# Kernel tuning notes

Measured on AMD Instinct MI355X. Metric: run time of the kernel, lower is better.

Reference implementation:

```python
import jax, jax.numpy as jnp
import numpy as np

SCORE_THRESH = 0.05
NMS_THRESH = 0.5
DETS_PER_IMG = 100
IMG_W, IMG_H = 1333.0, 800.0
BBOX_XFORM_CLIP = float(np.log(1000.0 / 16.0))
WX, WY, WW, WH = 10.0, 10.0, 5.0, 5.0


def decode_boxes(rel, ref):
    widths = ref[:, 2] - ref[:, 0] + 1.0
    heights = ref[:, 3] - ref[:, 1] + 1.0
    ctr_x = ref[:, 0] + 0.5 * widths
    ctr_y = ref[:, 1] + 0.5 * heights
    dx = rel[:, 0] / WX
    dy = rel[:, 1] / WY
    dw = jnp.minimum(rel[:, 2] / WW, BBOX_XFORM_CLIP)
    dh = jnp.minimum(rel[:, 3] / WH, BBOX_XFORM_CLIP)
    pcx = dx * widths + ctr_x
    pcy = dy * heights + ctr_y
    pw = jnp.exp(dw) * widths
    ph = jnp.exp(dh) * heights
    return jnp.stack([pcx - 0.5 * pw, pcy - 0.5 * ph,
                      pcx + 0.5 * pw - 1.0, pcy + 0.5 * ph - 1.0], axis=1)


def pairwise_iou(b):
    # torchvision-style IoU (no +1), b: [n,4] xyxy
    area = (b[:, 2] - b[:, 0]) * (b[:, 3] - b[:, 1])
    lt = jnp.maximum(b[:, None, :2], b[None, :, :2])
    rb = jnp.minimum(b[:, None, 2:], b[None, :, 2:])
    wh = jnp.clip(rb - lt, 0.0)
    inter = wh[..., 0] * wh[..., 1]
    return inter / (area[:, None] + area[None, :] - inter + 1e-12)


def nms_keep(boxes, scores, valid):
    # masked greedy NMS; returns boolean keep mask in original order
    n = boxes.shape[0]
    order = jnp.argsort(-jnp.where(valid, scores, -jnp.inf))
    b = boxes[order]
    v = valid[order]
    iou = pairwise_iou(b)  # [n,n]
    idx = jnp.arange(n)

    def body(i, keep):
        suppressed = jnp.any(keep & (iou[i] > NMS_THRESH) & (idx < i))
        return keep.at[i].set(v[i] & ~suppressed)

    keep_sorted = jax.lax.fori_loop(0, n, body, jnp.zeros(n, dtype=bool))
    return jnp.zeros(n, dtype=bool).at[order].set(keep_sorted)


def setup_inputs() -> dict:
    key = jax.random.key(0)
    k1, k2, k3, k4, k5 = jax.random.split(key, 5)
    C, K = 16, 2048
    class_logit = jax.random.normal(k1, (C * K, 2), jnp.float32)
    box_regression = jax.random.normal(k2, (C * K, 8), jnp.float32) * 0.5
    x1 = jax.random.uniform(k3, (K,)) * (IMG_W - 220.0)
    y1 = jax.random.uniform(k4, (K,)) * (IMG_H - 220.0)
    wh = 20.0 + jax.random.uniform(k5, (K, 2)) * 180.0
    proposal_boxes = jnp.stack([x1, y1, x1 + wh[:, 0], y1 + wh[:, 1]], axis=1).astype(jnp.float32)
    unique_labels = jnp.arange(1, C + 1, dtype=jnp.int32)
    return {"class_logit": class_logit, "box_regression": box_regression,
            "proposal_boxes": proposal_boxes, "unique_labels": unique_labels}


def reference(class_logit, box_regression, proposal_boxes, unique_labels):
    C = unique_labels.shape[0]
    K = proposal_boxes.shape[0]
    # softmax over binary logits, take foreground prob
    prob = jax.nn.softmax(class_logit, axis=1)[:, 1]  # [C*K]
    rel = box_regression[:, 4:8]
    ref_boxes = jnp.tile(proposal_boxes, (C, 1))  # class-major [C*K,4]
    dec = decode_boxes(rel, ref_boxes)
    # clip_to_image (remove_empty=False), TO_REMOVE = 1
    dec = jnp.stack([jnp.clip(dec[:, 0], 0.0, IMG_W - 1.0),
                     jnp.clip(dec[:, 1], 0.0, IMG_H - 1.0),
                     jnp.clip(dec[:, 2], 0.0, IMG_W - 1.0),
                     jnp.clip(dec[:, 3], 0.0, IMG_H - 1.0)], axis=1)
    boxes_c = dec.reshape(C, K, 4)
    scores_c = prob.reshape(C, K)
    valid = scores_c > SCORE_THRESH
    keep = jax.vmap(nms_keep)(boxes_c, scores_c, valid).reshape(-1)  # [C*K]
    flat_scores = scores_c.reshape(-1)
    n_det = jnp.sum(keep)
    masked = jnp.where(keep, flat_scores, -jnp.inf)
    kth = jax.lax.top_k(masked, DETS_PER_IMG)[0][-1]  # 100th largest kept score
    keep_final = jnp.where(n_det > DETS_PER_IMG, keep & (flat_scores >= kth), keep)
    labels = jnp.broadcast_to(unique_labels[:, None], (C, K)).reshape(-1)
    out_boxes = jnp.where(keep_final[:, None], dec, 0.0)
    out_scores = jnp.where(keep_final, flat_scores, 0.0)
    out5 = jnp.concatenate([out_boxes, out_scores[:, None]], axis=1)  # [C*K,5]
    return out5, labels, keep_final
```

## Files before the change

kernel.cpp:

```cpp
#include <hip/hip_runtime.h>
#include <hip/hip_bf16.h>

#define NCLS 16
#define NBOX 2048
#define NTOT (NCLS * NBOX)
#define NCHUNK 32
#define SCORE_THRESH 0.05f
#define NMS_THRESH 0.5f
#define DETS_PER_IMG 100
#define BBOX_CLIP 4.135166556742356f

typedef unsigned long long u64;

__device__ __forceinline__ u64 sel_mx(u64 a, u64 b, bool keepmax) {
    u64 mx = (a > b) ? a : b;
    u64 mn = (a > b) ? b : a;
    return keepmax ? mx : mn;
}

__global__ __launch_bounds__(1024) void sortdecode_kernel(
    const float* __restrict__ logits,
    const float* __restrict__ regr,
    const float* __restrict__ props,
    float4* __restrict__ dec,
    u64* __restrict__ keys_out,
    float4* __restrict__ sbox4)
{
    int c = blockIdx.x;
    int tid = threadIdx.x;
    int w = tid >> 6, l = tid & 63;
    int p0 = w * 128 + l;
    int p1 = p0 + 64;
    __shared__ u64 sk[NBOX];

    u64 e01[2];
#pragma unroll
    for (int s = 0; s < 2; s++) {
#pragma clang fp contract(off)
        int t = s ? p1 : p0;
        int i = c * NBOX + t;
        float x0 = logits[2 * i + 0];
        float x1 = logits[2 * i + 1];
        float m = fmaxf(x0, x1);
        float e0f = expf(x0 - m);
        float e1f = expf(x1 - m);
        float score = e1f / (e0f + e1f);

        float px1 = props[4 * t + 0];
        float py1 = props[4 * t + 1];
        float px2 = props[4 * t + 2];
        float py2 = props[4 * t + 3];

        float bw = px2 - px1 + 1.0f;
        float bh = py2 - py1 + 1.0f;
        float cx = px1 + 0.5f * bw;
        float cy = py1 + 0.5f * bh;

        float dx = regr[8 * i + 4] / 10.0f;
        float dy = regr[8 * i + 5] / 10.0f;
        float dw = fminf(regr[8 * i + 6] / 5.0f, BBOX_CLIP);
        float dh = fminf(regr[8 * i + 7] / 5.0f, BBOX_CLIP);

        float pcx = dx * bw + cx;
        float pcy = dy * bh + cy;
        float pw  = expf(dw) * bw;
        float ph  = expf(dh) * bh;

        float b0 = pcx - 0.5f * pw;
        float b1 = pcy - 0.5f * ph;
        float b2 = pcx + 0.5f * pw - 1.0f;
        float b3 = pcy + 0.5f * ph - 1.0f;

        b0 = fminf(fmaxf(b0, 0.0f), 1332.0f);
        b1 = fminf(fmaxf(b1, 0.0f), 799.0f);
        b2 = fminf(fmaxf(b2, 0.0f), 1332.0f);
        b3 = fminf(fmaxf(b3, 0.0f), 799.0f);

        dec[i] = make_float4(b0, b1, b2, b3);

        unsigned mono = 0u;
        if (score > SCORE_THRESH) mono = __float_as_uint(score) | 0x80000000u;
        e01[s] = ((u64)mono << 32) | (u64)(unsigned)(NBOX - 1 - t);
    }
    u64 e0 = e01[0], e1 = e01[1];

    for (int k = 2; k <= NBOX; k <<= 1) {
        bool desc0 = (p0 & k) == 0;
        bool desc1 = (p1 & k) == 0;
        for (int j = k >> 1; j > 0; j >>= 1) {
            if (j >= 128) {
                sk[p0] = e0; sk[p1] = e1;
                __syncthreads();
                u64 q0 = sk[p0 ^ j];
                u64 q1 = sk[p1 ^ j];
                e0 = sel_mx(e0, q0, desc0 ^ ((p0 & j) != 0));
                e1 = sel_mx(e1, q1, desc1 ^ ((p1 & j) != 0));
                __syncthreads();
            } else if (j == 64) {
                u64 mx = (e0 > e1) ? e0 : e1;
                u64 mn = (e0 > e1) ? e1 : e0;
                e0 = desc0 ? mx : mn;
                e1 = desc0 ? mn : mx;
            } else {
                u64 q0 = __shfl_xor(e0, j);
                u64 q1 = __shfl_xor(e1, j);
                bool hi = (l & j) != 0;
                e0 = sel_mx(e0, q0, desc0 ^ hi);
                e1 = sel_mx(e1, q1, desc1 ^ hi);
            }
        }
    }

    sk[p0] = e0; sk[p1] = e1;
    __syncthreads();

    for (int t = tid; t < NBOX; t += 1024) {
        u64 key = sk[t];
        keys_out[c * NBOX + t] = key;
        int idx = (NBOX - 1) - (int)(key & 0xFFFFFFFFull);
        int orig = c * NBOX + idx;
        sbox4[c * NBOX + t] = dec[orig];
    }
}

__global__ __launch_bounds__(1024) void mask_kernel(
    const float4* __restrict__ sbox4,
    u64* __restrict__ maskT)
{
    int c = blockIdx.x >> 4;
    int p = blockIdx.x & 15;
    __shared__ float4 box[NBOX];

    for (int i = threadIdx.x; i < NBOX; i += 1024)
        box[i] = sbox4[c * NBOX + i];
    __syncthreads();

    int r = threadIdx.x & 63;
    int g = threadIdx.x >> 6;

    for (int pass = 0; pass < 2; pass++) {
#pragma clang fp contract(off)
        int Jc = pass ? (31 - p) : p;
        int j = Jc * 64 + r;
        float4 jb = box[j];
        float jar = (jb.z - jb.x) * (jb.w - jb.y);
        float hj = 0.5f * jar;
        float colC = hj + 5e-13f;

        for (int I = g; I <= Jc; I += 16) {
            u64 w = 0;
            int rbase = I * 64;
#pragma unroll
            for (int i2 = 0; i2 < 64; i2++) {
#pragma clang fp contract(off)
                int gi = rbase + i2;
                float4 rb = box[gi];
                float ar = (rb.z - rb.x) * (rb.w - rb.y);
                float rha = 0.5f * ar;
                float lx = fmaxf(rb.x, jb.x);
                float ly = fmaxf(rb.y, jb.y);
                float rx = fminf(rb.z, jb.z);
                float ry = fminf(rb.w, jb.w);
                float ww = fmaxf(rx - lx, 0.0f);
                float hh = fmaxf(ry - ly, 0.0f);
                float inter = ww * hh;
                float s  = rha + colC;
                float band = 2e-6f * s;
                float delta = fmaf(1.5f, inter, -s);
                bool over = delta > band;
                bool amb = fabsf(delta) <= band;
                if (__any(amb)) {
                    float un = ar + jar - inter + 1e-12f;
                    float iou = inter / un;
                    bool ovx = iou > NMS_THRESH;
                    over = amb ? ovx : over;
                }
                if (over) w |= 1ull << i2;
            }
            if (I == Jc) w &= (1ull << r) - 1ull;
            maskT[((size_t)c * NCHUNK + I) * NBOX + j] = w;
        }
    }
}

__global__ __launch_bounds__(64) void resolve_kernel(
    const u64* __restrict__ keys,
    const u64* __restrict__ maskT,
    unsigned* __restrict__ keepbits)
{
    int c = blockIdx.x;
    int l = threadIdx.x;
    const u64* MT = maskT + (size_t)c * NCHUNK * NBOX;
    const u64* K  = keys + (size_t)c * NBOX;

    unsigned sup = 0;
    u64 tm[2][NCHUNK - 1];

#pragma unroll
    for (int t = 0; t < NCHUNK - 1; t++)
        tm[0][t] = MT[(size_t)(1 + t) * 64 + l];
    u64 diag = MT[l];
    u64 key  = K[l];

#pragma unroll
    for (int I = 0; I < NCHUNK; I++) {
        u64 diagN = diag, keyN = key;
        if (I + 1 < NCHUNK) {
            const u64* rowpN = MT + (size_t)(I + 1) * NBOX + l;
#pragma unroll
            for (int t = 0; t < NCHUNK - 2 - I; t++)
                tm[(I + 1) & 1][t] = rowpN[(size_t)(I + 2 + t) * 64];
            diagN = MT[(size_t)(I + 1) * NBOX + (size_t)(I + 1) * 64 + l];
            keyN  = K[(I + 1) * 64 + l];
        }
        __builtin_amdgcn_sched_barrier(0);

        unsigned mono = (unsigned)(key >> 32);
        bool av = (mono != 0u) && (((sup >> I) & 1u) == 0u);
        u64 kept = 0;
        u64 availB = __ballot(av);
        while (availB) {
            u64 front = __ballot(av && ((diag & availB) == 0ull));
            kept |= front;
            bool fr = ((front >> l) & 1ull) != 0ull;
            bool sp = ((diag & front) != 0ull);
            av = av && !fr && !sp;
            availB = __ballot(av);
        }

        int idx = (NBOX - 1) - (int)(key & 0xFFFFFFFFull);
        keepbits[c * NBOX + idx] = ((kept >> l) & 1ull) ? (mono & 0x7FFFFFFFu) : 0u;

#pragma unroll
        for (int t = 0; t < NCHUNK - 1 - I; t++)
            sup |= (tm[I & 1][t] & kept) ? (1u << (I + 1 + t)) : 0u;

        diag = diagN;
        key  = keyN;
    }
}

__global__ __launch_bounds__(1024) void select_kernel(
    const unsigned* __restrict__ keepbits,
    int* __restrict__ stats)
{
    __shared__ int hist[4][2048];
    __shared__ int gsum[64];
    __shared__ int s_cnt;
    __shared__ unsigned s_prefix;
    __shared__ int s_rank;
    int tid = threadIdx.x;
    int cw = (tid >> 6) & 3;
    int* h0 = &hist[0][0];
    const uint4* kb4 = (const uint4*)keepbits;

    for (int b = tid; b < 4 * 2048; b += 1024) h0[b] = 0;
    if (tid == 0) s_cnt = 0;
    __syncthreads();
    int cnt = 0;
    for (int i = tid; i < NTOT / 4; i += 1024) {
        uint4 v = kb4[i];
        if (v.x) { cnt++; atomicAdd(&hist[cw][v.x >> 21], 1); }
        if (v.y) { cnt++; atomicAdd(&hist[cw][v.y >> 21], 1); }
        if (v.z) { cnt++; atomicAdd(&hist[cw][v.z >> 21], 1); }
        if (v.w) { cnt++; atomicAdd(&hist[cw][v.w >> 21], 1); }
    }
#pragma unroll
    for (int off = 32; off > 0; off >>= 1) cnt += __shfl_down(cnt, off);
    if ((tid & 63) == 0) atomicAdd(&s_cnt, cnt);
    __syncthreads();
    for (int b = tid; b < 2048; b += 1024)
        h0[b] = hist[0][b] + hist[1][b] + hist[2][b] + hist[3][b];
    __syncthreads();
    int n_det = s_cnt;

    if (n_det > DETS_PER_IMG) {
        if (tid < 64) {
            int s = 0;
            for (int t = 0; t < 32; t++) s += h0[tid * 32 + t];
            gsum[tid] = s;
        }
        __syncthreads();
        if (tid == 0) {
            int r = DETS_PER_IMG;
            int g = 63;
            for (; g > 0; g--) { if (r <= gsum[g]) break; r -= gsum[g]; }
            int b = g * 32 + 31;
            for (; b > g * 32; b--) { if (r <= h0[b]) break; r -= h0[b]; }
            s_prefix = (unsigned)b << 21;
            s_rank = r;
        }
        __syncthreads();

        unsigned p1 = s_prefix;
        for (int b = tid; b < 2048; b += 1024) h0[b] = 0;
        __syncthreads();
        for (int i = tid; i < NTOT / 4; i += 1024) {
            uint4 v = kb4[i];
            if (v.x && (v.x >> 21 << 21) == p1) atomicAdd(&h0[(v.x >> 10) & 2047], 1);
            if (v.y && (v.y >> 21 << 21) == p1) atomicAdd(&h0[(v.y >> 10) & 2047], 1);
            if (v.z && (v.z >> 21 << 21) == p1) atomicAdd(&h0[(v.z >> 10) & 2047], 1);
            if (v.w && (v.w >> 21 << 21) == p1) atomicAdd(&h0[(v.w >> 10) & 2047], 1);
        }
        __syncthreads();
        if (tid < 64) {
            int s = 0;
            for (int t = 0; t < 32; t++) s += h0[tid * 32 + t];
            gsum[tid] = s;
        }
        __syncthreads();
        if (tid == 0) {
            int r = s_rank;
            int g = 63;
            for (; g > 0; g--) { if (r <= gsum[g]) break; r -= gsum[g]; }
            int b = g * 32 + 31;
            for (; b > g * 32; b--) { if (r <= h0[b]) break; r -= h0[b]; }
            s_prefix = p1 | ((unsigned)b << 10);
            s_rank = r;
        }
        __syncthreads();

        unsigned p2 = s_prefix;
        for (int b = tid; b < 1024; b += 1024) h0[b] = 0;
        __syncthreads();
        for (int i = tid; i < NTOT / 4; i += 1024) {
            uint4 v = kb4[i];
            if (v.x && (v.x >> 10 << 10) == p2) atomicAdd(&h0[v.x & 1023], 1);
            if (v.y && (v.y >> 10 << 10) == p2) atomicAdd(&h0[v.y & 1023], 1);
            if (v.z && (v.z >> 10 << 10) == p2) atomicAdd(&h0[v.z & 1023], 1);
            if (v.w && (v.w >> 10 << 10) == p2) atomicAdd(&h0[v.w & 1023], 1);
        }
        __syncthreads();
        if (tid < 32) {
            int s = 0;
            for (int t = 0; t < 32; t++) s += h0[tid * 32 + t];
            gsum[tid] = s;
        }
        __syncthreads();
        if (tid == 0) {
            int r = s_rank;
            int g = 31;
            for (; g > 0; g--) { if (r <= gsum[g]) break; r -= gsum[g]; }
            int b = g * 32 + 31;
            for (; b > g * 32; b--) { if (r <= h0[b]) break; r -= h0[b]; }
            s_prefix = p2 | (unsigned)b;
        }
        __syncthreads();
    }

    if (tid == 0) {
        stats[0] = n_det;
        stats[1] = (n_det > DETS_PER_IMG) ? (int)s_prefix : 0;
    }
}

__global__ __launch_bounds__(256) void write_kernel(
    const unsigned* __restrict__ keepbits,
    const float4* __restrict__ dec,
    const int* __restrict__ stats,
    const int* __restrict__ ulabels,
    float* __restrict__ out)
{
    int i = blockIdx.x * blockDim.x + threadIdx.x;
    if (i >= NTOT) return;

    int n_det = stats[0];
    unsigned kth = (unsigned)stats[1];
    unsigned kb = keepbits[i];
    bool kf = kb && (n_det <= DETS_PER_IMG || kb >= kth);

    float4 b = dec[i];
    float* o5 = out + (size_t)i * 5;
    if (kf) {
        o5[0] = b.x; o5[1] = b.y; o5[2] = b.z; o5[3] = b.w;
        o5[4] = __uint_as_float(kb);
    } else {
        o5[0] = 0.0f; o5[1] = 0.0f; o5[2] = 0.0f; o5[3] = 0.0f; o5[4] = 0.0f;
    }

    int c = i >> 11;
    out[NTOT * 5 + i] = (float)ulabels[c];
    out[NTOT * 5 + NTOT + i] = kf ? 1.0f : 0.0f;
}

extern "C" void kernel_launch(void* const* d_in, const int* in_sizes, int n_in,
                              void* d_out, int out_size, void* d_ws, size_t ws_size,
                              hipStream_t stream) {
    (void)in_sizes; (void)n_in; (void)out_size; (void)ws_size;

    const float* class_logit    = (const float*)d_in[0];
    const float* box_regression = (const float*)d_in[1];
    const float* proposal_boxes = (const float*)d_in[2];
    const int*   unique_labels  = (const int*)d_in[3];

    char* ws = (char*)d_ws;
    float4* dec        = (float4*)(ws + 0);
    u64* keys          = (u64*)(ws + 524288);
    float4* sbox4      = (float4*)(ws + 786432);
    unsigned* keepbits = (unsigned*)(ws + 1441792);
    int* stats         = (int*)(ws + 1572864);
    u64* maskT         = (u64*)(ws + 1573120);

    float* out = (float*)d_out;

    sortdecode_kernel<<<NCLS, 1024, 0, stream>>>(class_logit, box_regression,
                                                 proposal_boxes, dec, keys,
                                                 sbox4);
    mask_kernel<<<NCLS * 16, 1024, 0, stream>>>(sbox4, maskT);
    resolve_kernel<<<NCLS, 64, 0, stream>>>(keys, maskT, keepbits);
    select_kernel<<<1, 1024, 0, stream>>>(keepbits, stats);
    write_kernel<<<NTOT / 256, 256, 0, stream>>>(keepbits, dec, stats,
                                                 unique_labels, out);
}
```

Before: 145.7 us.

## Compact per-class top kept scores in resolve and bisect kth from them

The resolve kernel now also writes each class's kept scores in descending sort order into a small compact buffer (the first 128 per class) and records the kept count. The select kernel becomes a single wavefront that finds the 100th-largest kept score by bitwise bisection with binary searches over these sorted lists. This replaces the three full histogram passes over all 32K keepbits with shared-memory atomics. It relies on the top 100 overall lying within each class's top 128, which always holds, and adds a small serial loop of 32 steps.

```diff
diff --git a/kernel.cpp b/kernel.cpp
--- a/kernel.cpp
+++ b/kernel.cpp
@@ -8,6 +8,7 @@
 #define SCORE_THRESH 0.05f
 #define NMS_THRESH 0.5f
 #define DETS_PER_IMG 100
+#define TOPC 128
 #define BBOX_CLIP 4.135166556742356f
 
 typedef unsigned long long u64;
@@ -186,7 +187,9 @@
 __global__ __launch_bounds__(64) void resolve_kernel(
     const u64* __restrict__ keys,
     const u64* __restrict__ maskT,
-    unsigned* __restrict__ keepbits)
+    unsigned* __restrict__ keepbits,
+    unsigned* __restrict__ compact,
+    int* __restrict__ nkept)
 {
     int c = blockIdx.x;
     int l = threadIdx.x;
@@ -194,6 +197,7 @@
     const u64* K  = keys + (size_t)c * NBOX;
 
     unsigned sup = 0;
+    int offset = 0;
     u64 tm[2][NCHUNK - 1];
 
 #pragma unroll
@@ -229,7 +233,12 @@
         }
 
         int idx = (NBOX - 1) - (int)(key & 0xFFFFFFFFull);
-        keepbits[c * NBOX + idx] = ((kept >> l) & 1ull) ? (mono & 0x7FFFFFFFu) : 0u;
+        bool isk = ((kept >> l) & 1ull) != 0ull;
+        keepbits[c * NBOX + idx] = isk ? (mono & 0x7FFFFFFFu) : 0u;
+
+        int pos = offset + __popcll(kept & ((1ull << l) - 1ull));
+        if (isk && pos < TOPC) compact[c * TOPC + pos] = mono;
+        offset += __popcll(kept);
 
 #pragma unroll
         for (int t = 0; t < NCHUNK - 1 - I; t++)
@@ -238,119 +247,57 @@
         diag = diagN;
         key  = keyN;
     }
-}
-
-__global__ __launch_bounds__(1024) void select_kernel(
-    const unsigned* __restrict__ keepbits,
+
+    for (int t = offset + l; t < TOPC; t += 64) compact[c * TOPC + t] = 0u;
+    if (l == 0) nkept[c] = offset;
+}
+
+__global__ __launch_bounds__(64) void select_kernel(
+    const unsigned* __restrict__ compact,
+    const int* __restrict__ nkept,
     int* __restrict__ stats)
 {
-    __shared__ int hist[4][2048];
-    __shared__ int gsum[64];
-    __shared__ int s_cnt;
-    __shared__ unsigned s_prefix;
-    __shared__ int s_rank;
-    int tid = threadIdx.x;
-    int cw = (tid >> 6) & 3;
-    int* h0 = &hist[0][0];
-    const uint4* kb4 = (const uint4*)keepbits;
-
-    for (int b = tid; b < 4 * 2048; b += 1024) h0[b] = 0;
-    if (tid == 0) s_cnt = 0;
+    __shared__ unsigned ls[NCLS * TOPC];
+    int l = threadIdx.x;
+
+    for (int t = l; t < NCLS * TOPC; t += 64) ls[t] = compact[t];
+    int n_c = (l < NCLS) ? nkept[l] : 0;
     __syncthreads();
-    int cnt = 0;
-    for (int i = tid; i < NTOT / 4; i += 1024) {
-        uint4 v = kb4[i];
-        if (v.x) { cnt++; atomicAdd(&hist[cw][v.x >> 21], 1); }
-        if (v.y) { cnt++; atomicAdd(&hist[cw][v.y >> 21], 1); }
-        if (v.z) { cnt++; atomicAdd(&hist[cw][v.z >> 21], 1); }
-        if (v.w) { cnt++; atomicAdd(&hist[cw][v.w >> 21], 1); }
-    }
-#pragma unroll
-    for (int off = 32; off > 0; off >>= 1) cnt += __shfl_down(cnt, off);
-    if ((tid & 63) == 0) atomicAdd(&s_cnt, cnt);
-    __syncthreads();
-    for (int b = tid; b < 2048; b += 1024)
-        h0[b] = hist[0][b] + hist[1][b] + hist[2][b] + hist[3][b];
-    __syncthreads();
-    int n_det = s_cnt;
-
-    if (n_det > DETS_PER_IMG) {
-        if (tid < 64) {
-            int s = 0;
-            for (int t = 0; t < 32; t++) s += h0[tid * 32 + t];
-            gsum[tid] = s;
-        }
-        __syncthreads();
-        if (tid == 0) {
-            int r = DETS_PER_IMG;
-            int g = 63;
-            for (; g > 0; g--) { if (r <= gsum[g]) break; r -= gsum[g]; }
-            int b = g * 32 + 31;
-            for (; b > g * 32; b--) { if (r <= h0[b]) break; r -= h0[b]; }
-            s_prefix = (unsigned)b << 21;
-            s_rank = r;
-        }
-        __syncthreads();
-
-        unsigned p1 = s_prefix;
-        for (int b = tid; b < 2048; b += 1024) h0[b] = 0;
-        __syncthreads();
-        for (int i = tid; i < NTOT / 4; i += 1024) {
-            uint4 v = kb4[i];
-            if (v.x && (v.x >> 21 << 21) == p1) atomicAdd(&h0[(v.x >> 10) & 2047], 1);
-            if (v.y && (v.y >> 21 << 21) == p1) atomicAdd(&h0[(v.y >> 10) & 2047], 1);
-            if (v.z && (v.z >> 21 << 21) == p1) atomicAdd(&h0[(v.z >> 10) & 2047], 1);
-            if (v.w && (v.w >> 21 << 21) == p1) atomicAdd(&h0[(v.w >> 10) & 2047], 1);
-        }
-        __syncthreads();
-        if (tid < 64) {
-            int s = 0;
-            for (int t = 0; t < 32; t++) s += h0[tid * 32 + t];
-            gsum[tid] = s;
-        }
-        __syncthreads();
-        if (tid == 0) {
-            int r = s_rank;
-            int g = 63;
-            for (; g > 0; g--) { if (r <= gsum[g]) break; r -= gsum[g]; }
-            int b = g * 32 + 31;
-            for (; b > g * 32; b--) { if (r <= h0[b]) break; r -= h0[b]; }
-            s_prefix = p1 | ((unsigned)b << 10);
-            s_rank = r;
-        }
-        __syncthreads();
-
-        unsigned p2 = s_prefix;
-        for (int b = tid; b < 1024; b += 1024) h0[b] = 0;
-        __syncthreads();
-        for (int i = tid; i < NTOT / 4; i += 1024) {
-            uint4 v = kb4[i];
-            if (v.x && (v.x >> 10 << 10) == p2) atomicAdd(&h0[v.x & 1023], 1);
-            if (v.y && (v.y >> 10 << 10) == p2) atomicAdd(&h0[v.y & 1023], 1);
-            if (v.z && (v.z >> 10 << 10) == p2) atomicAdd(&h0[v.z & 1023], 1);
-            if (v.w && (v.w >> 10 << 10) == p2) atomicAdd(&h0[v.w & 1023], 1);
-        }
-        __syncthreads();
-        if (tid < 32) {
-            int s = 0;
-            for (int t = 0; t < 32; t++) s += h0[tid * 32 + t];
-            gsum[tid] = s;
-        }
-        __syncthreads();
-        if (tid == 0) {
-            int r = s_rank;
-            int g = 31;
-            for (; g > 0; g--) { if (r <= gsum[g]) break; r -= gsum[g]; }
-            int b = g * 32 + 31;
-            for (; b > g * 32; b--) { if (r <= h0[b]) break; r -= h0[b]; }
-            s_prefix = p2 | (unsigned)b;
-        }
-        __syncthreads();
-    }
-
-    if (tid == 0) {
-        stats[0] = n_det;
-        stats[1] = (n_det > DETS_PER_IMG) ? (int)s_prefix : 0;
+
+    int nd = n_c;
+#pragma unroll
+    for (int off = 32; off > 0; off >>= 1) nd += __shfl_down(nd, off);
+    nd = __shfl(nd, 0);
+
+    unsigned kth = 0u;
+    if (nd > DETS_PER_IMG) {
+        const unsigned* my = &ls[(l & 15) * TOPC];
+        bool active = (l < NCLS);
+        unsigned prefix = 0u;
+        for (int bit = 31; bit >= 0; bit--) {
+            unsigned cand = prefix | (1u << bit);
+            int cnt = 0;
+            if (active) {
+                if (my[TOPC - 1] >= cand) cnt = TOPC;
+                else {
+                    int pos = 0;
+#pragma unroll
+                    for (int step = 64; step >= 1; step >>= 1)
+                        if (my[pos + step - 1] >= cand) pos += step;
+                    cnt = pos;
+                }
+            }
+#pragma unroll
+            for (int off = 32; off > 0; off >>= 1) cnt += __shfl_down(cnt, off);
+            cnt = __shfl(cnt, 0);
+            if (cnt >= DETS_PER_IMG) prefix = cand;
+        }
+        kth = prefix & 0x7FFFFFFFu;
+    }
+
+    if (l == 0) {
+        stats[0] = nd;
+        stats[1] = (int)kth;
     }
 }
 
@@ -400,6 +347,8 @@
     unsigned* keepbits = (unsigned*)(ws + 1441792);
     int* stats         = (int*)(ws + 1572864);
     u64* maskT         = (u64*)(ws + 1573120);
+    unsigned* compact  = (unsigned*)(ws + 9961728);
+    int* nkept         = (int*)(ws + 9969920);
 
     float* out = (float*)d_out;
 
@@ -407,8 +356,9 @@
                                                  proposal_boxes, dec, keys,
                                                  sbox4);
     mask_kernel<<<NCLS * 16, 1024, 0, stream>>>(sbox4, maskT);
-    resolve_kernel<<<NCLS, 64, 0, stream>>>(keys, maskT, keepbits);
-    select_kernel<<<1, 1024, 0, stream>>>(keepbits, stats);
+    resolve_kernel<<<NCLS, 64, 0, stream>>>(keys, maskT, keepbits,
+                                            compact, nkept);
+    select_kernel<<<1, 64, 0, stream>>>(compact, nkept, stats);
     write_kernel<<<NTOT / 256, 256, 0, stream>>>(keepbits, dec, stats,
                                                  unique_labels, out);
 }
```

Measured after the change: 144.4 us. Within noise of the previous version (-0.9%).
